# Optimization experiments

Hardware: AMD Instinct MI355X
Metric: run time of the kernel (lower is better)

## Reference

```python
import jax, jax.numpy as jnp
import numpy as np

BATCH = 4096
DIM = 512
TEMP = 0.1

def setup_inputs() -> dict:
    key = jax.random.key(0)
    k1, k2 = jax.random.split(key)
    emb_i = jax.random.normal(k1, (BATCH, DIM), dtype=jnp.float32)
    emb_j = jax.random.normal(k2, (BATCH, DIM), dtype=jnp.float32)
    return {"emb_i": emb_i, "emb_j": emb_j}

def _l2_normalize(x, eps=1e-12):
    # matches torch F.normalize(dim=1): x / max(||x||, eps)
    norm = jnp.sqrt(jnp.sum(x * x, axis=1, keepdims=True))
    return x / jnp.maximum(norm, eps)

def reference(emb_i, emb_j):
    n = emb_i.shape[0]
    z_i = _l2_normalize(emb_i)
    z_j = _l2_normalize(emb_j)
    reps = jnp.concatenate([z_i, z_j], axis=0)  # [2N, D], rows unit-norm
    # cosine similarity of unit vectors == dot product -> GEMM instead of O(N^2 D) broadcast
    sim = reps @ reps.T  # [2N, 2N]
    # positives: diag offsets +N and -N
    pos_ij = jnp.sum(z_i * z_j, axis=1)  # diag(sim, +N)
    pos_ji = pos_ij                      # diag(sim, -N) is identical by symmetry
    positives = jnp.concatenate([pos_ij, pos_ji], axis=0)  # [2N]
    nominator = jnp.exp(positives / TEMP)
    neg_mask = 1.0 - jnp.eye(2 * n, dtype=sim.dtype)
    denominator = jnp.sum(neg_mask * jnp.exp(sim / TEMP), axis=1)  # [2N]
    loss_partial = -jnp.log(nominator / denominator)
    return jnp.sum(loss_partial) / (2 * n)
```

## Files before the change

### kernel.cpp

```cpp
#include <hip/hip_runtime.h>
#include <hip/hip_bf16.h>

#define N_ROWS 4096
#define DIM    512
#define M_ROWS 8192
#define BK     32
#define EXP_SCALE 14.4269504088896340736f

typedef unsigned short ushort_t;
typedef __attribute__((ext_vector_type(8))) short short8;
typedef __attribute__((ext_vector_type(4))) float f32x4;

__device__ __forceinline__ ushort_t f2bf(float x) {
  unsigned int bits = __float_as_uint(x);
  unsigned int lsb = (bits >> 16) & 1u;
  bits += 0x7fffu + lsb;
  return (ushort_t)(bits >> 16);
}

__device__ __forceinline__ void store4bf(ushort_t* p, float4 v, float s) {
  union { ushort_t u[4]; uint2 d; } pk;
  pk.u[0] = f2bf(v.x * s);
  pk.u[1] = f2bf(v.y * s);
  pk.u[2] = f2bf(v.z * s);
  pk.u[3] = f2bf(v.w * s);
  *(uint2*)p = pk.d;
}

__device__ __forceinline__ void async16(const ushort_t* g, ushort_t* l) {
  __builtin_amdgcn_global_load_lds(
      (const __attribute__((address_space(1))) void*)g,
      (__attribute__((address_space(3))) void*)l,
      16, 0, 0);
}

__global__ __launch_bounds__(64) void norm_kernel(
    const float* __restrict__ ei, const float* __restrict__ ej,
    ushort_t* __restrict__ reps, float* __restrict__ pos) {
  int b = blockIdx.x;
  int lane = threadIdx.x;
  const float4* pi = (const float4*)(ei + (size_t)b * DIM);
  const float4* pj = (const float4*)(ej + (size_t)b * DIM);
  float4 a0 = pi[lane];
  float4 a1 = pi[lane + 64];
  float4 b0 = pj[lane];
  float4 b1 = pj[lane + 64];

  float si = a0.x*a0.x + a0.y*a0.y + a0.z*a0.z + a0.w*a0.w
           + a1.x*a1.x + a1.y*a1.y + a1.z*a1.z + a1.w*a1.w;
  float sj = b0.x*b0.x + b0.y*b0.y + b0.z*b0.z + b0.w*b0.w
           + b1.x*b1.x + b1.y*b1.y + b1.z*b1.z + b1.w*b1.w;
  float dp = a0.x*b0.x + a0.y*b0.y + a0.z*b0.z + a0.w*b0.w
           + a1.x*b1.x + a1.y*b1.y + a1.z*b1.z + a1.w*b1.w;

#pragma unroll
  for (int m = 32; m >= 1; m >>= 1) {
    si += __shfl_xor(si, m, 64);
    sj += __shfl_xor(sj, m, 64);
    dp += __shfl_xor(dp, m, 64);
  }
  float ii = 1.0f / fmaxf(sqrtf(si), 1e-12f);
  float ij = 1.0f / fmaxf(sqrtf(sj), 1e-12f);
  if (lane == 0) pos[b] = dp * ii * ij;

  ushort_t* ri = reps + (size_t)b * DIM;
  ushort_t* rj = reps + (size_t)(b + N_ROWS) * DIM;
  store4bf(ri + lane * 4,       a0, ii);
  store4bf(ri + 256 + lane * 4, a1, ii);
  store4bf(rj + lane * 4,       b0, ij);
  store4bf(rj + 256 + lane * 4, b1, ij);
}

__global__ __launch_bounds__(256) void sim_kernel(
    const ushort_t* __restrict__ reps, float* __restrict__ denom) {
  int bj = blockIdx.x, bi = blockIdx.y;
  if (bi > bj) return;

  __shared__ ushort_t As[128 * BK];
  __shared__ ushort_t Bs[128 * BK];

  int tid  = threadIdx.x;
  int wave = tid >> 6, lane = tid & 63;
  int wr = wave >> 1, wc = wave & 1;
  int quad = lane >> 4, l15 = lane & 15;

  int c0 = wave * 2, c1 = c0 + 1;
  int srow  = lane >> 2;
  int selem = (lane & 3) * 8;
  const ushort_t* gA0 = reps + (size_t)(bi * 128 + c0 * 16 + srow) * DIM + selem;
  const ushort_t* gA1 = reps + (size_t)(bi * 128 + c1 * 16 + srow) * DIM + selem;
  const ushort_t* gB0 = reps + (size_t)(bj * 128 + c0 * 16 + srow) * DIM + selem;
  const ushort_t* gB1 = reps + (size_t)(bj * 128 + c1 * 16 + srow) * DIM + selem;
  ushort_t* lA0 = As + c0 * 512;
  ushort_t* lA1 = As + c1 * 512;
  ushort_t* lB0 = Bs + c0 * 512;
  ushort_t* lB1 = Bs + c1 * 512;

  f32x4 zero4 = {0.0f, 0.0f, 0.0f, 0.0f};
  f32x4 acc[4][4];
#pragma unroll
  for (int tr = 0; tr < 4; ++tr)
#pragma unroll
    for (int tc = 0; tc < 4; ++tc) acc[tr][tc] = zero4;

  for (int kk = 0; kk < DIM; kk += BK) {
    __syncthreads();
    async16(gA0 + kk, lA0);
    async16(gA1 + kk, lA1);
    async16(gB0 + kk, lB0);
    async16(gB1 + kk, lB1);
    __syncthreads();

    short8 aF[4], bF[4];
#pragma unroll
    for (int t = 0; t < 4; ++t) {
      aF[t] = *(const short8*)(As + (wr * 64 + t * 16 + l15) * BK + quad * 8);
      bF[t] = *(const short8*)(Bs + (wc * 64 + t * 16 + l15) * BK + quad * 8);
    }
#pragma unroll
    for (int tr = 0; tr < 4; ++tr)
#pragma unroll
      for (int tc = 0; tc < 4; ++tc)
        acc[tr][tc] = __builtin_amdgcn_mfma_f32_16x16x32_bf16(
            aF[tr], bF[tc], acc[tr][tc], 0, 0, 0);
  }

  int rowg_base = bi * 128 + wr * 64;
  int colg_base = bj * 128 + wc * 64;

  f32x4 rsum[4];
  float csum[4] = {0.0f, 0.0f, 0.0f, 0.0f};
#pragma unroll
  for (int tr = 0; tr < 4; ++tr) rsum[tr] = zero4;

#pragma unroll
  for (int tr = 0; tr < 4; ++tr) {
    int rowg0 = rowg_base + tr * 16 + quad * 4;
#pragma unroll
    for (int tc = 0; tc < 4; ++tc) {
      int colg = colg_base + tc * 16 + l15;
      f32x4 a = acc[tr][tc];
      f32x4 e;
#pragma unroll
      for (int r = 0; r < 4; ++r) {
        float v = exp2f(a[r] * EXP_SCALE);
        e[r] = ((rowg0 + r) == colg) ? 0.0f : v;
      }
      rsum[tr] += e;
      csum[tc] += e[0] + e[1] + e[2] + e[3];
    }
  }

#pragma unroll
  for (int m = 1; m <= 8; m <<= 1)
#pragma unroll
    for (int tr = 0; tr < 4; ++tr)
#pragma unroll
      for (int r = 0; r < 4; ++r)
        rsum[tr][r] += __shfl_xor(rsum[tr][r], m, 64);

  if (l15 == 0) {
#pragma unroll
    for (int tr = 0; tr < 4; ++tr)
#pragma unroll
      for (int r = 0; r < 4; ++r)
        atomicAdd(&denom[rowg_base + tr * 16 + quad * 4 + r], rsum[tr][r]);
  }

  if (bi != bj) {
#pragma unroll
    for (int m = 16; m <= 32; m <<= 1)
#pragma unroll
      for (int tc = 0; tc < 4; ++tc)
        csum[tc] += __shfl_xor(csum[tc], m, 64);
    if (quad == 0) {
#pragma unroll
      for (int tc = 0; tc < 4; ++tc)
        atomicAdd(&denom[colg_base + tc * 16 + l15], csum[tc]);
    }
  }
}

__global__ __launch_bounds__(256) void loss_kernel(
    const float* __restrict__ denom, const float* __restrict__ pos,
    float* __restrict__ out) {
  __shared__ float red[4];
  int tid = threadIdx.x;
  float p = 0.0f;
  for (int r = tid; r < M_ROWS; r += 256)
    p += logf(denom[r]) - pos[r & (N_ROWS - 1)] * 10.0f;
#pragma unroll
  for (int m = 32; m >= 1; m >>= 1) p += __shfl_xor(p, m, 64);
  if ((tid & 63) == 0) red[tid >> 6] = p;
  __syncthreads();
  if (tid == 0)
    out[0] = (red[0] + red[1] + red[2] + red[3]) * (1.0f / M_ROWS);
}

extern "C" void kernel_launch(void* const* d_in, const int* in_sizes, int n_in,
                              void* d_out, int out_size, void* d_ws, size_t ws_size,
                              hipStream_t stream) {
  const float* ei = (const float*)d_in[0];
  const float* ej = (const float*)d_in[1];
  float* out = (float*)d_out;

  char* ws = (char*)d_ws;
  ushort_t* reps = (ushort_t*)ws;
  float* denom = (float*)(ws + (size_t)M_ROWS * DIM * 2);
  float* pos = (float*)(ws + (size_t)M_ROWS * DIM * 2 + M_ROWS * 4);

  hipMemsetAsync(denom, 0, M_ROWS * sizeof(float), stream);
  norm_kernel<<<N_ROWS, 64, 0, stream>>>(ei, ej, reps, pos);
  sim_kernel<<<dim3(64, 64), 256, 0, stream>>>(reps, denom);
  loss_kernel<<<1, 256, 0, stream>>>(denom, pos, out);
}
```

Baseline: 156.9 us.

## Double-buffer LDS tiles, swizzle layout, compact triangular grid, fold memset into norm

Loads the next K-slice into a second LDS buffer while MFMAs run on the current one, which removes one barrier per iteration. LDS columns are XOR-swizzled to cut bank conflicts on the fragment reads. The 64x64 grid, half of whose blocks exited at once, becomes a linear launch of 2080 upper-triangle blocks, with index interleaving and a sqrt-based decode. The denominator zeroing moves into norm_kernel so the separate memset disappears. The cost is double the LDS footprint and the index-decode arithmetic.

```diff
diff --git a/kernel.cpp b/kernel.cpp
--- a/kernel.cpp
+++ b/kernel.cpp
@@ -1,10 +1,13 @@
 #include <hip/hip_runtime.h>
 #include <hip/hip_bf16.h>
+#include <math.h>
 
 #define N_ROWS 4096
 #define DIM    512
 #define M_ROWS 8192
 #define BK     32
+#define NTILES 64
+#define NBLOCKS 2080
 #define EXP_SCALE 14.4269504088896340736f
 
 typedef unsigned short ushort_t;
@@ -36,9 +39,14 @@
 
 __global__ __launch_bounds__(64) void norm_kernel(
     const float* __restrict__ ei, const float* __restrict__ ej,
-    ushort_t* __restrict__ reps, float* __restrict__ pos) {
+    ushort_t* __restrict__ reps, float* __restrict__ pos,
+    float* __restrict__ denom) {
   int b = blockIdx.x;
   int lane = threadIdx.x;
+  if (lane == 0) {
+    denom[b] = 0.0f;
+    denom[b + N_ROWS] = 0.0f;
+  }
   const float4* pi = (const float4*)(ei + (size_t)b * DIM);
   const float4* pj = (const float4*)(ej + (size_t)b * DIM);
   float4 a0 = pi[lane];
@@ -73,11 +81,15 @@
 
 __global__ __launch_bounds__(256) void sim_kernel(
     const ushort_t* __restrict__ reps, float* __restrict__ denom) {
-  int bj = blockIdx.x, bi = blockIdx.y;
-  if (bi > bj) return;
-
-  __shared__ ushort_t As[128 * BK];
-  __shared__ ushort_t Bs[128 * BK];
+  int id = blockIdx.x;
+  id = (id & 7) * (NBLOCKS / 8) + (id >> 3);
+  int bj = (int)((sqrtf(8.0f * (float)id + 1.0f) - 1.0f) * 0.5f);
+  while ((bj + 1) * (bj + 2) / 2 <= id) ++bj;
+  while (bj * (bj + 1) / 2 > id) --bj;
+  int bi = id - bj * (bj + 1) / 2;
+
+  __shared__ ushort_t As[2][128 * BK];
+  __shared__ ushort_t Bs[2][128 * BK];
 
   int tid  = threadIdx.x;
   int wave = tid >> 6, lane = tid & 63;
@@ -86,15 +98,11 @@
 
   int c0 = wave * 2, c1 = c0 + 1;
   int srow  = lane >> 2;
-  int selem = (lane & 3) * 8;
+  int selem = ((lane & 3) ^ ((srow >> 1) & 3)) * 8;
   const ushort_t* gA0 = reps + (size_t)(bi * 128 + c0 * 16 + srow) * DIM + selem;
   const ushort_t* gA1 = reps + (size_t)(bi * 128 + c1 * 16 + srow) * DIM + selem;
   const ushort_t* gB0 = reps + (size_t)(bj * 128 + c0 * 16 + srow) * DIM + selem;
   const ushort_t* gB1 = reps + (size_t)(bj * 128 + c1 * 16 + srow) * DIM + selem;
-  ushort_t* lA0 = As + c0 * 512;
-  ushort_t* lA1 = As + c1 * 512;
-  ushort_t* lB0 = Bs + c0 * 512;
-  ushort_t* lB1 = Bs + c1 * 512;
 
   f32x4 zero4 = {0.0f, 0.0f, 0.0f, 0.0f};
   f32x4 acc[4][4];
@@ -103,19 +111,29 @@
 #pragma unroll
     for (int tc = 0; tc < 4; ++tc) acc[tr][tc] = zero4;
 
+  int sqr = (quad ^ ((l15 >> 1) & 3)) * 8;
+
+  async16(gA0, &As[0][c0 * 512]);
+  async16(gA1, &As[0][c1 * 512]);
+  async16(gB0, &Bs[0][c0 * 512]);
+  async16(gB1, &Bs[0][c1 * 512]);
+  __syncthreads();
+
+  int cur = 0;
   for (int kk = 0; kk < DIM; kk += BK) {
-    __syncthreads();
-    async16(gA0 + kk, lA0);
-    async16(gA1 + kk, lA1);
-    async16(gB0 + kk, lB0);
-    async16(gB1 + kk, lB1);
-    __syncthreads();
+    int nxt = cur ^ 1;
+    if (kk + BK < DIM) {
+      async16(gA0 + kk + BK, &As[nxt][c0 * 512]);
+      async16(gA1 + kk + BK, &As[nxt][c1 * 512]);
+      async16(gB0 + kk + BK, &Bs[nxt][c0 * 512]);
+      async16(gB1 + kk + BK, &Bs[nxt][c1 * 512]);
+    }
 
     short8 aF[4], bF[4];
 #pragma unroll
     for (int t = 0; t < 4; ++t) {
-      aF[t] = *(const short8*)(As + (wr * 64 + t * 16 + l15) * BK + quad * 8);
-      bF[t] = *(const short8*)(Bs + (wc * 64 + t * 16 + l15) * BK + quad * 8);
+      aF[t] = *(const short8*)(&As[cur][(wr * 64 + t * 16 + l15) * BK + sqr]);
+      bF[t] = *(const short8*)(&Bs[cur][(wc * 64 + t * 16 + l15) * BK + sqr]);
     }
 #pragma unroll
     for (int tr = 0; tr < 4; ++tr)
@@ -123,6 +141,9 @@
       for (int tc = 0; tc < 4; ++tc)
         acc[tr][tc] = __builtin_amdgcn_mfma_f32_16x16x32_bf16(
             aF[tr], bF[tc], acc[tr][tc], 0, 0, 0);
+
+    __syncthreads();
+    cur = nxt;
   }
 
   int rowg_base = bi * 128 + wr * 64;
@@ -209,8 +230,7 @@
   float* denom = (float*)(ws + (size_t)M_ROWS * DIM * 2);
   float* pos = (float*)(ws + (size_t)M_ROWS * DIM * 2 + M_ROWS * 4);
 
-  hipMemsetAsync(denom, 0, M_ROWS * sizeof(float), stream);
-  norm_kernel<<<N_ROWS, 64, 0, stream>>>(ei, ej, reps, pos);
-  sim_kernel<<<dim3(64, 64), 256, 0, stream>>>(reps, denom);
+  norm_kernel<<<N_ROWS, 64, 0, stream>>>(ei, ej, reps, pos, denom);
+  sim_kernel<<<NBLOCKS, 256, 0, stream>>>(reps, denom);
   loss_kernel<<<1, 256, 0, stream>>>(denom, pos, out);
 }
```

After: 146.2 us. 1.07x faster.
